# Kernel optimization log

Hardware: AMD Instinct MI355X
Metric: run time of the kernel (lower is better)

## Reference

```python
import jax, jax.numpy as jnp
import numpy as np

NP_, NA_ = 50000, 20000
D_IN, D_HID, D_OUT = 128, 128, 64
E_W, E_C, E_R = 250000, 500000, 250000


def setup_inputs() -> dict:
    key = jax.random.key(0)
    ks = jax.random.split(key, 14)
    s_in = 1.0 / np.sqrt(D_IN)
    s_h = 1.0 / np.sqrt(D_HID)
    return {
        "x_paper": jax.random.normal(ks[0], (NP_, D_IN), jnp.float32),
        "x_author": jax.random.normal(ks[1], (NA_, D_IN), jnp.float32),
        "Wl1": jax.random.normal(ks[2], (3, D_HID, D_IN), jnp.float32) * s_in,
        "bl1": jax.random.normal(ks[3], (3, D_HID), jnp.float32) * 0.01,
        "Wr1": jax.random.normal(ks[4], (3, D_HID, D_IN), jnp.float32) * s_in,
        "Wl2": jax.random.normal(ks[5], (3, D_OUT, D_HID), jnp.float32) * s_h,
        "bl2": jax.random.normal(ks[6], (3, D_OUT), jnp.float32) * 0.01,
        "Wr2": jax.random.normal(ks[7], (3, D_OUT, D_HID), jnp.float32) * s_h,
        "writes_src": jax.random.randint(ks[8], (E_W,), 0, NA_),
        "writes_dst": jax.random.randint(ks[9], (E_W,), 0, NP_),
        "cites_src": jax.random.randint(ks[10], (E_C,), 0, NP_),
        "cites_dst": jax.random.randint(ks[11], (E_C,), 0, NP_),
        "rev_src": jax.random.randint(ks[12], (E_R,), 0, NP_),
        "rev_dst": jax.random.randint(ks[13], (E_R,), 0, NA_),
    }


def _sage(x_src, x_dst, src, dst, Wl, bl, Wr, n_dst):
    # PyG SAGEConv(aggr='mean'): lin_l(mean_j x_src[j]) + lin_r(x_dst)
    agg = jax.ops.segment_sum(x_src[src], dst, num_segments=n_dst)
    cnt = jax.ops.segment_sum(jnp.ones_like(dst, dtype=x_src.dtype), dst,
                              num_segments=n_dst)
    agg = agg / jnp.maximum(cnt, 1.0)[:, None]  # degree-0 nodes -> 0 (PyG scatter-mean)
    return agg @ Wl.T + bl + x_dst @ Wr.T


def reference(x_paper, x_author, Wl1, bl1, Wr1, Wl2, bl2, Wr2,
              writes_src, writes_dst, cites_src, cites_dst, rev_src, rev_dst):
    def hetero_layer(xp, xa, Wl, bl, Wr):
        # HeteroConv(aggr='mean'): average per-relation outputs per dst node type
        op = 0.5 * (_sage(xa, xp, writes_src, writes_dst, Wl[0], bl[0], Wr[0], NP_)
                    + _sage(xp, xp, cites_src, cites_dst, Wl[1], bl[1], Wr[1], NP_))
        oa = _sage(xp, xa, rev_src, rev_dst, Wl[2], bl[2], Wr[2], NA_)
        return op, oa

    hp, ha = hetero_layer(x_paper, x_author, Wl1, bl1, Wr1)
    hp, ha = jax.nn.relu(hp), jax.nn.relu(ha)  # norm_type='none', dropout eval-mode
    hp, _ = hetero_layer(hp, ha, Wl2, bl2, Wr2)
    return hp  # logits for category='paper', [NP_, D_OUT]
```

## Files before the change

### kernel.cpp

```cpp
#include <hip/hip_runtime.h>

#define NP 50000
#define NA 20000
#define E_W 250000
#define E_C 500000
#define E_R 250000
#define E_TOT (E_W + E_C + E_R)
#define CAP 48
#define RBLK 4096
#define NSEG 245
#define PNODES 15000
#define CHK 125
#define NCH 120
#define NBIN 960

typedef __attribute__((ext_vector_type(8))) short short8;
typedef __attribute__((ext_vector_type(4))) float floatx4;
typedef __attribute__((ext_vector_type(2))) float floatx2;

__device__ __forceinline__ unsigned short f2bf(float f) {
    unsigned u = __float_as_uint(f);
    return (unsigned short)((u + 0x7FFFu + ((u >> 16) & 1u)) >> 16);
}
__device__ __forceinline__ float bflo(unsigned v) { return __uint_as_float(v << 16); }
__device__ __forceinline__ float bfhi(unsigned v) { return __uint_as_float(v & 0xFFFF0000u); }

__device__ __forceinline__ int frag_off(int NT, int j, int n, int k) {
    int t = n >> 4, ln = n & 15;
    int kb = k >> 5, q = (k >> 3) & 3, r = k & 7;
    return (((j * NT + t) * 4 + kb) * 64 + q * 16 + ln) * 8 + r;
}

__device__ __forceinline__ void prep_body(
    int idx,
    const float* __restrict__ xp, const float* __restrict__ xa,
    const float* __restrict__ Wl1, const float* __restrict__ Wr1,
    const float* __restrict__ Wl2, const float* __restrict__ Wr2,
    const float* __restrict__ bl1, const float* __restrict__ bl2,
    unsigned short* __restrict__ xpb, unsigned short* __restrict__ xab,
    unsigned* __restrict__ xp8, unsigned* __restrict__ xa8,
    unsigned short* __restrict__ Wp1, unsigned short* __restrict__ Wa1,
    unsigned short* __restrict__ Wt2, unsigned short* __restrict__ Wr2s,
    float* __restrict__ bias_p1, float* __restrict__ bias_a1,
    float* __restrict__ bias_p2) {
    const int n4p = NP * 32, n4a = NA * 32;
    if (idx < n4p + n4a) {
        const float* s; unsigned short* d; unsigned* d8; int i = idx;
        if (i < n4p) { s = xp; d = xpb; d8 = xp8; }
        else { s = xa; d = xab; d8 = xa8; i -= n4p; }
        float4 v = ((const float4*)s)[i];
        ushort4 u;
        u.x = f2bf(v.x); u.y = f2bf(v.y); u.z = f2bf(v.z); u.w = f2bf(v.w);
        ((ushort4*)d)[i] = u;
        int w = __builtin_amdgcn_cvt_pk_fp8_f32(v.x, v.y, 0, false);
        w = __builtin_amdgcn_cvt_pk_fp8_f32(v.z, v.w, w, true);
        d8[i] = (unsigned)w;
        return;
    }
    int j = idx - (n4p + n4a);
    if (j < 49152) {
        int jj = j >> 14, rem = j & 16383, n = rem >> 7, k = rem & 127;
        float v = (jj == 0)   ? 0.5f * Wl1[rem]
                  : (jj == 1) ? 0.5f * Wl1[16384 + rem]
                              : 0.5f * (Wr1[rem] + Wr1[16384 + rem]);
        Wp1[frag_off(8, jj, n, k)] = f2bf(v);
    } else if (j < 81920) {
        int i2 = j - 49152;
        int jj = i2 >> 14, rem = i2 & 16383, n = rem >> 7, k = rem & 127;
        float v = (jj == 0) ? Wl1[2 * 16384 + rem] : Wr1[2 * 16384 + rem];
        Wa1[frag_off(8, jj, n, k)] = f2bf(v);
    } else if (j < 98304) {
        int i2 = j - 81920;
        int jj = i2 >> 13, rem = i2 & 8191, n = rem >> 7, k = rem & 127;
        float v = 0.5f * Wl2[jj * 8192 + rem];
        Wt2[frag_off(4, jj, n, k)] = f2bf(v);
    } else if (j < 106496) {
        int i2 = j - 98304;
        int n = i2 >> 7, k = i2 & 127;
        float v = 0.5f * (Wr2[i2] + Wr2[8192 + i2]);
        Wr2s[frag_off(4, 0, n, k)] = f2bf(v);
    } else if (j < 106496 + 320) {
        int b = j - 106496;
        if (b < 128) bias_p1[b] = 0.5f * (bl1[b] + bl1[128 + b]);
        else if (b < 256) bias_a1[b - 128] = bl1[256 + b - 128];
        else bias_p2[b - 256] = 0.5f * (bl2[b - 256] + bl2[64 + b - 256]);
    }
}

__device__ __forceinline__ void edge_bin(
    int e, const int* __restrict__ w_src, const int* __restrict__ w_dst,
    const int* __restrict__ c_src, const int* __restrict__ c_dst,
    const int* __restrict__ r_src, const int* __restrict__ r_dst,
    int& bin, int& sub, int& src) {
    bool isC = (e >= E_W) & (e < E_W + E_C);
    bool isR = e >= E_W + E_C;
    const int* db = isR ? r_dst : (isC ? c_dst : w_dst);
    const int* sb = isR ? r_src : (isC ? c_src : w_src);
    int idx = e - (isC ? E_W : 0) - (isR ? (E_W + E_C) : 0);
    int d = db[idx];
    src = sb[idx];
    int p, local;
    if (isR) { p = d / 2500; local = 12500 + d - p * 2500; }
    else { p = d / 6250; local = (d - p * 6250) + (isC ? 6250 : 0); }
    int ch = local / CHK;
    bin = p * NCH + ch;
    sub = local - ch * CHK;
}

__device__ __forceinline__ void route_body(
    int bid, const int* __restrict__ w_src, const int* __restrict__ w_dst,
    const int* __restrict__ c_src, const int* __restrict__ c_dst,
    const int* __restrict__ r_src, const int* __restrict__ r_dst,
    unsigned* __restrict__ seg, int* __restrict__ segoff, int* __restrict__ segcnt,
    int* cnt_s, int* base_s, int* cur_s) {
    int tid = threadIdx.x, lane = tid & 63;
    for (int k = tid; k < NBIN; k += 256) cnt_s[k] = 0;
    __syncthreads();
#pragma unroll 4
    for (int u = 0; u < 16; ++u) {
        int e = bid * RBLK + u * 256 + tid;
        if (e < E_TOT) {
            int bin, sub, src;
            edge_bin(e, w_src, w_dst, c_src, c_dst, r_src, r_dst, bin, sub, src);
            atomicAdd(&cnt_s[bin], 1);
        }
    }
    __syncthreads();
    if (tid < 64) {
        int v[15], tot = 0;
#pragma unroll
        for (int q = 0; q < 15; ++q) {
            v[q] = cnt_s[tid * 15 + q];
            tot += v[q];
        }
        int sc = tot;
#pragma unroll
        for (int ofs = 1; ofs < 64; ofs <<= 1) {
            int t = __shfl_up(sc, ofs, 64);
            if (lane >= ofs) sc += t;
        }
        int run = sc - tot;
#pragma unroll
        for (int q = 0; q < 15; ++q) {
            base_s[tid * 15 + q] = run;
            run += v[q];
        }
    }
    __syncthreads();
    for (int k = tid; k < NBIN; k += 256) {
        segoff[bid * NBIN + k] = base_s[k];
        segcnt[bid * NBIN + k] = cnt_s[k];
        cur_s[k] = base_s[k];
    }
    __syncthreads();
    unsigned* segb = seg + (size_t)bid * RBLK;
#pragma unroll 4
    for (int u = 0; u < 16; ++u) {
        int e = bid * RBLK + u * 256 + tid;
        if (e < E_TOT) {
            int bin, sub, src;
            edge_bin(e, w_src, w_dst, c_src, c_dst, r_src, r_dst, bin, sub, src);
            int pos = atomicAdd(&cur_s[bin], 1);
            segb[pos] = (unsigned)src | ((unsigned)sub << 16);
        }
    }
}

__global__ __launch_bounds__(256) void route_prep(
    const float* xp, const float* xa, const float* Wl1, const float* Wr1,
    const float* Wl2, const float* Wr2, const float* bl1, const float* bl2,
    unsigned short* xpb, unsigned short* xab, unsigned* xp8, unsigned* xa8,
    unsigned short* Wp1, unsigned short* Wa1, unsigned short* Wt2, unsigned short* Wr2s,
    float* bias_p1, float* bias_a1, float* bias_p2,
    const int* w_src, const int* w_dst, const int* c_src, const int* c_dst,
    const int* r_src, const int* r_dst,
    unsigned* seg, int* segoff, int* segcnt) {
    __shared__ int cnt_s[NBIN], base_s[NBIN], cur_s[NBIN];
    if ((int)blockIdx.x < NSEG)
        route_body(blockIdx.x, w_src, w_dst, c_src, c_dst, r_src, r_dst,
                   seg, segoff, segcnt, cnt_s, base_s, cur_s);
    else
        prep_body((blockIdx.x - NSEG) * 256 + threadIdx.x, xp, xa, Wl1, Wr1, Wl2, Wr2,
                  bl1, bl2, xpb, xab, xp8, xa8, Wp1, Wa1, Wt2, Wr2s,
                  bias_p1, bias_a1, bias_p2);
}

__global__ __launch_bounds__(512) void fill_agg(
    const unsigned* __restrict__ seg, const int* __restrict__ segoff,
    const int* __restrict__ segcnt, int* __restrict__ cnt,
    unsigned short* __restrict__ csr,
    const unsigned* __restrict__ xp8, const unsigned* __restrict__ xa8,
    unsigned short* __restrict__ aggP1, unsigned short* __restrict__ aggP2,
    unsigned short* __restrict__ aggA) {
    __shared__ __align__(16) unsigned short rows[CHK * CAP];
    __shared__ int cursor[CHK];
    __shared__ int offs[NSEG], cnts[NSEG];
    int tid = threadIdx.x;
    int b = blockIdx.x, p, ch;
    if (b < 160)      { p = b / 20;  ch = 100 + b % 20; }
    else if (b < 560) { int t = b - 160; p = t / 50; ch = 50 + t % 50; }
    else              { int t = b - 560; p = t / 50; ch = t % 50; }
    int k = p * NCH + ch;
    for (int s = tid; s < NSEG; s += 512) {
        offs[s] = segoff[s * NBIN + k];
        cnts[s] = segcnt[s * NBIN + k];
    }
    for (int l = tid; l < CHK; l += 512) cursor[l] = 0;
    __syncthreads();
    int grp = tid >> 4, gl = tid & 15;
    for (int s = grp; s < NSEG; s += 32) {
        int n = cnts[s];
        const unsigned* sp = seg + (size_t)s * RBLK + offs[s];
        for (int i = gl; i < n; i += 16) {
            unsigned v = sp[i];
            int sub = v >> 16, src = v & 0xFFFFu;
            int pos = atomicAdd(&cursor[sub], 1);
            if (pos < CAP) rows[sub * CAP + pos] = (unsigned short)src;
        }
    }
    __syncthreads();
    if (ch < 100) {
        int gbase = p * PNODES + ch * CHK;
        for (int l = tid; l < CHK; l += 512) cnt[gbase + l] = cursor[l];
        const unsigned* rU = (const unsigned*)rows;
        unsigned* cU = (unsigned*)csr + (size_t)gbase * (CAP / 2);
        for (int i = tid; i < CHK * (CAP / 2); i += 512) cU[i] = rU[i];
    }
    const unsigned* src8; unsigned short* dst; int nodebase, dummy;
    if (ch < 50)       { src8 = xa8; dst = aggP1; nodebase = p * 6250 + ch * CHK;         dummy = NA; }
    else if (ch < 100) { src8 = xp8; dst = aggP2; nodebase = p * 6250 + (ch - 50) * CHK;  dummy = NP; }
    else               { src8 = xp8; dst = aggA;  nodebase = p * 2500 + (ch - 100) * CHK; dummy = NP; }
    int g = tid >> 5, sl = tid & 31;
    for (int l = g; l < CHK; l += 16) {
        int deg = cursor[l];
        int degc = deg < CAP ? deg : CAP;
        float a0 = 0.f, a1 = 0.f, a2 = 0.f, a3 = 0.f;
        float b0 = 0.f, b1 = 0.f, b2 = 0.f, b3 = 0.f;
        for (int i = 0; i < degc; i += 8) {
            short8 rr = *(const short8*)&rows[l * CAP + i];
            unsigned v[8];
#pragma unroll
            for (int u = 0; u < 8; ++u) {
                int ii = i + u;
                int q = (ii < degc) ? (int)(unsigned short)rr[u] : dummy;
                v[u] = src8[(q << 5) + sl];
            }
#pragma unroll
            for (int u = 0; u < 8; ++u) {
                floatx2 lo = __builtin_amdgcn_cvt_pk_f32_fp8(v[u], false);
                floatx2 hi = __builtin_amdgcn_cvt_pk_f32_fp8(v[u], true);
                if (u & 1) { b0 += lo.x; b1 += lo.y; b2 += hi.x; b3 += hi.y; }
                else       { a0 += lo.x; a1 += lo.y; a2 += hi.x; a3 += hi.y; }
            }
        }
        float scl = deg > 0 ? 1.f / (float)deg : 0.f;
        float r0 = (a0 + b0) * scl, r1 = (a1 + b1) * scl;
        float r2 = (a2 + b2) * scl, r3 = (a3 + b3) * scl;
        unsigned wlo = ((unsigned)f2bf(r1) << 16) | (unsigned)f2bf(r0);
        unsigned whi = ((unsigned)f2bf(r3) << 16) | (unsigned)f2bf(r2);
        ((uint2*)dst)[((nodebase + l) << 5) + sl] = make_uint2(wlo, whi);
    }
}

__global__ void agg2(const unsigned short* __restrict__ ta, const unsigned short* __restrict__ tp,
                     const int* __restrict__ cnt, const unsigned short* __restrict__ csr,
                     const float* __restrict__ sp_in, const float* __restrict__ bias_p2,
                     float* __restrict__ out) {
    int node = blockIdx.x * 8 + (threadIdx.x >> 5);
    if (node >= NP) return;
    int lane = threadIdx.x & 63;
    int sl = lane & 31;
    int hw = lane & 32;
    int p2 = node / 6250;
    int base = p2 * PNODES + (node - p2 * 6250);
    float r0 = 0.f, r1 = 0.f;
#pragma unroll
    for (int rel = 0; rel < 2; ++rel) {
        int dummy = (rel == 0) ? NA : NP;
        const unsigned* sp = (const unsigned*)((rel == 0) ? ta : tp);
        int idx = base + (rel ? 6250 : 0);
        int deg = cnt[idx];
        int degc = deg < CAP ? deg : CAP;
        const unsigned short* row = csr + (size_t)idx * CAP;
        int ei0 = (sl < degc) ? (int)row[sl] : dummy;
        int ei1 = (32 + sl < degc) ? (int)row[32 + sl] : dummy;
        int degw = degc;
        int other = __shfl_xor(degw, 32, 64);
        if (other > degw) degw = other;
        float s0 = 0.f, s1 = 0.f, t0 = 0.f, t1 = 0.f;
        for (int i = 0; i < degw; i += 8) {
            unsigned v[8];
#pragma unroll
            for (int u = 0; u < 8; ++u) {
                int ii = i + u;
                int esrc = (ii < 32) ? ei0 : ei1;
                int qq = __shfl(esrc, hw | (ii & 31), 64);
                qq = (ii < degc) ? qq : dummy;
                v[u] = sp[(qq << 5) + sl];
            }
#pragma unroll
            for (int u = 0; u < 8; ++u) {
                if (u & 1) { t0 += bflo(v[u]); t1 += bfhi(v[u]); }
                else       { s0 += bflo(v[u]); s1 += bfhi(v[u]); }
            }
        }
        float scl = deg > 0 ? 1.f / (float)deg : 0.f;
        r0 += (s0 + t0) * scl; r1 += (s1 + t1) * scl;
    }
    float2 spv = ((const float2*)sp_in)[(size_t)node * 32 + sl];
    float2 bv = ((const float2*)bias_p2)[sl];
    ((float2*)out)[(size_t)node * 32 + sl] =
        make_float2(r0 + spv.x + bv.x, r1 + spv.y + bv.y);
}

template <int J, bool SP>
__device__ __forceinline__ void l1_core(
    const unsigned short* __restrict__ A0, const unsigned short* __restrict__ A1,
    const unsigned short* __restrict__ A2, const unsigned short* __restrict__ Wf,
    const float* __restrict__ bias,
    const unsigned short* __restrict__ Wt, unsigned short* __restrict__ tout,
    const unsigned short* __restrict__ Wsp, float* __restrict__ spout,
    unsigned short (*hT)[136], int M, int blk) {
    int tid = threadIdx.x;
    int wave = tid >> 6, lane = tid & 63;
    int ln = lane & 15, quad = lane >> 4;
    int row = blk * 64 + wave * 16 + ln;
    int rowc = row < M ? row : M - 1;
    const unsigned short* As[3] = {A0, A1, A2};
    floatx4 acc[8];
#pragma unroll
    for (int t = 0; t < 8; ++t) acc[t] = (floatx4){0.f, 0.f, 0.f, 0.f};
#pragma unroll
    for (int j = 0; j < J; ++j) {
        const unsigned short* A = As[j] + (long)rowc * 128 + quad * 8;
        const unsigned short* Wj = Wf + j * (128 * 128) + lane * 8;
#pragma unroll
        for (int kb = 0; kb < 4; ++kb) {
            short8 af = *(const short8*)(A + kb * 32);
#pragma unroll
            for (int t = 0; t < 8; ++t) {
                short8 bf = *(const short8*)(Wj + (t * 4 + kb) * 512);
                acc[t] = __builtin_amdgcn_mfma_f32_16x16x32_bf16(af, bf, acc[t], 0, 0, 0);
            }
        }
    }
    int orow0 = blk * 64 + wave * 16 + quad * 4;
    int lrow0 = wave * 16 + quad * 4;
#pragma unroll
    for (int t = 0; t < 8; ++t) {
        int col = t * 16 + ln;
        float bv = bias[col];
#pragma unroll
        for (int r = 0; r < 4; ++r) {
            float v = fmaxf(acc[t][r] + bv, 0.f);
            hT[lrow0 + r][col] = f2bf(v);
        }
    }
    __syncthreads();
    floatx4 tacc[4], sacc[4];
#pragma unroll
    for (int t = 0; t < 4; ++t) {
        tacc[t] = (floatx4){0.f, 0.f, 0.f, 0.f};
        sacc[t] = (floatx4){0.f, 0.f, 0.f, 0.f};
    }
#pragma unroll
    for (int kb = 0; kb < 4; ++kb) {
        short8 af = *(const short8*)&hT[wave * 16 + ln][quad * 8 + kb * 32];
#pragma unroll
        for (int t = 0; t < 4; ++t) {
            short8 bf = *(const short8*)(Wt + (t * 4 + kb) * 512 + lane * 8);
            tacc[t] = __builtin_amdgcn_mfma_f32_16x16x32_bf16(af, bf, tacc[t], 0, 0, 0);
            if (SP) {
                short8 bs = *(const short8*)(Wsp + (t * 4 + kb) * 512 + lane * 8);
                sacc[t] = __builtin_amdgcn_mfma_f32_16x16x32_bf16(af, bs, sacc[t], 0, 0, 0);
            }
        }
    }
#pragma unroll
    for (int t = 0; t < 4; ++t) {
        int col = t * 16 + ln;
#pragma unroll
        for (int r = 0; r < 4; ++r) {
            int orow = orow0 + r;
            if (orow < M) {
                tout[(long)orow * 64 + col] = f2bf(tacc[t][r]);
                if (SP) spout[(long)orow * 64 + col] = sacc[t][r];
            }
        }
    }
}

__global__ __launch_bounds__(256) void gemm_l1f(
    const unsigned short* aggP1, const unsigned short* aggP2, const unsigned short* xpb,
    const unsigned short* Wp1, const float* bias_p1,
    const unsigned short* aggA, const unsigned short* xab,
    const unsigned short* Wa1, const float* bias_a1,
    const unsigned short* Wt2, const unsigned short* Wr2s,
    unsigned short* ta, unsigned short* tp, float* sp) {
    __shared__ unsigned short hT[64][136];
    constexpr int PB = (NP + 63) / 64;
    if ((int)blockIdx.x < PB)
        l1_core<3, true>(aggP1, aggP2, xpb, Wp1, bias_p1, Wt2 + 64 * 128, tp, Wr2s, sp,
                         hT, NP, blockIdx.x);
    else
        l1_core<2, false>(aggA, xab, nullptr, Wa1, bias_a1, Wt2, ta, nullptr, nullptr,
                          hT, NA, blockIdx.x - PB);
}

extern "C" void kernel_launch(void* const* d_in, const int* in_sizes, int n_in,
                              void* d_out, int out_size, void* d_ws, size_t ws_size,
                              hipStream_t stream) {
    (void)in_sizes; (void)n_in; (void)out_size; (void)ws_size;
    const float* xp  = (const float*)d_in[0];
    const float* xa  = (const float*)d_in[1];
    const float* Wl1 = (const float*)d_in[2];
    const float* bl1 = (const float*)d_in[3];
    const float* Wr1 = (const float*)d_in[4];
    const float* Wl2 = (const float*)d_in[5];
    const float* bl2 = (const float*)d_in[6];
    const float* Wr2 = (const float*)d_in[7];
    const int* w_src = (const int*)d_in[8];
    const int* w_dst = (const int*)d_in[9];
    const int* c_src = (const int*)d_in[10];
    const int* c_dst = (const int*)d_in[11];
    const int* r_src = (const int*)d_in[12];
    const int* r_dst = (const int*)d_in[13];
    float* out = (float*)d_out;

    char* p = (char*)d_ws;
    auto alloc = [&](size_t bytes) {
        char* r = p;
        p += (bytes + 255) & ~(size_t)255;
        return r;
    };
    unsigned short* xpb   = (unsigned short*)alloc((size_t)NP * 128 * 2);
    unsigned short* xab   = (unsigned short*)alloc((size_t)NA * 128 * 2);
    unsigned*       xp8   = (unsigned*)alloc((size_t)(NP + 1) * 128);
    unsigned*       xa8   = (unsigned*)alloc((size_t)(NA + 1) * 128);
    unsigned short* aggP1 = (unsigned short*)alloc((size_t)NP * 128 * 2);
    unsigned short* aggP2 = (unsigned short*)alloc((size_t)NP * 128 * 2);
    unsigned short* aggA  = (unsigned short*)alloc((size_t)NA * 128 * 2);
    unsigned short* ta    = (unsigned short*)alloc((size_t)(NA + 1) * 64 * 2);
    unsigned short* tp    = (unsigned short*)alloc((size_t)(NP + 1) * 64 * 2);
    float*          sp    = (float*)alloc((size_t)NP * 64 * 4);
    int*            cnt    = (int*)alloc((size_t)8 * PNODES * 4);
    unsigned short* csr    = (unsigned short*)alloc((size_t)8 * PNODES * CAP * 2);
    unsigned*       seg    = (unsigned*)alloc((size_t)NSEG * RBLK * 4);
    int*            segoff = (int*)alloc((size_t)NSEG * NBIN * 4);
    int*            segcnt = (int*)alloc((size_t)NSEG * NBIN * 4);
    unsigned short* Wp1  = (unsigned short*)alloc(3 * 128 * 128 * 2);
    unsigned short* Wa1  = (unsigned short*)alloc(2 * 128 * 128 * 2);
    unsigned short* Wt2  = (unsigned short*)alloc(2 * 64 * 128 * 2);
    unsigned short* Wr2s = (unsigned short*)alloc(64 * 128 * 2);
    float* bias_p1 = (float*)alloc(128 * 4);
    float* bias_a1 = (float*)alloc(128 * 4);
    float* bias_p2 = (float*)alloc(64 * 4);

    hipMemsetAsync(xp8 + (size_t)NP * 32, 0, 128, stream);
    hipMemsetAsync(xa8 + (size_t)NA * 32, 0, 128, stream);
    hipMemsetAsync(ta + (size_t)NA * 64, 0, 128, stream);
    hipMemsetAsync(tp + (size_t)NP * 64, 0, 128, stream);

    int prep_threads = (NP + NA) * 32 + 106496 + 320;
    int prep_blocks = (prep_threads + 255) / 256;
    route_prep<<<NSEG + prep_blocks, 256, 0, stream>>>(
        xp, xa, Wl1, Wr1, Wl2, Wr2, bl1, bl2,
        xpb, xab, xp8, xa8, Wp1, Wa1, Wt2, Wr2s, bias_p1, bias_a1, bias_p2,
        w_src, w_dst, c_src, c_dst, r_src, r_dst, seg, segoff, segcnt);

    fill_agg<<<NBIN, 512, 0, stream>>>(seg, segoff, segcnt, cnt, csr,
                                       xp8, xa8, aggP1, aggP2, aggA);

    gemm_l1f<<<(NP + 63) / 64 + (NA + 63) / 64, 256, 0, stream>>>(
        aggP1, aggP2, xpb, Wp1, bias_p1, aggA, xab, Wa1, bias_a1, Wt2, Wr2s, ta, tp, sp);

    agg2<<<(NP + 7) / 8, 256, 0, stream>>>(ta, tp, cnt, csr, sp, bias_p2, out);
}
```

Baseline: 207.7 us.

## Fuse layer-1 neighbor gather with layer-1 GEMM and layer-2 projection per 64-node tile

```diff
diff --git a/kernel.cpp b/kernel.cpp
--- a/kernel.cpp
+++ b/kernel.cpp
@@ -9,10 +9,9 @@
 #define CAP 48
 #define RBLK 4096
 #define NSEG 245
-#define PNODES 15000
-#define CHK 125
-#define NCH 120
-#define NBIN 960
+#define NCHP 782
+#define NCHA 313
+#define NBIN (NCHP + NCHA)
 
 typedef __attribute__((ext_vector_type(8))) short short8;
 typedef __attribute__((ext_vector_type(4))) float floatx4;
@@ -99,12 +98,8 @@
     int idx = e - (isC ? E_W : 0) - (isR ? (E_W + E_C) : 0);
     int d = db[idx];
     src = sb[idx];
-    int p, local;
-    if (isR) { p = d / 2500; local = 12500 + d - p * 2500; }
-    else { p = d / 6250; local = (d - p * 6250) + (isC ? 6250 : 0); }
-    int ch = local / CHK;
-    bin = p * NCH + ch;
-    sub = local - ch * CHK;
+    if (isR) { bin = NCHP + (d >> 6); sub = d & 63; }
+    else { bin = d >> 6; sub = (d & 63) + (isC ? 64 : 0); }
 }
 
 __device__ __forceinline__ void route_body(
@@ -127,10 +122,11 @@
     }
     __syncthreads();
     if (tid < 64) {
-        int v[15], tot = 0;
-#pragma unroll
-        for (int q = 0; q < 15; ++q) {
-            v[q] = cnt_s[tid * 15 + q];
+        int v[18], tot = 0;
+#pragma unroll
+        for (int q = 0; q < 18; ++q) {
+            int k = tid * 18 + q;
+            v[q] = (k < NBIN) ? cnt_s[k] : 0;
             tot += v[q];
         }
         int sc = tot;
@@ -141,9 +137,9 @@
         }
         int run = sc - tot;
 #pragma unroll
-        for (int q = 0; q < 15; ++q) {
-            base_s[tid * 15 + q] = run;
-            run += v[q];
+        for (int q = 0; q < 18; ++q) {
+            int k = tid * 18 + q;
+            if (k < NBIN) { base_s[k] = run; run += v[q]; }
         }
     }
     __syncthreads();
@@ -185,80 +181,201 @@
                   bias_p1, bias_a1, bias_p2);
 }
 
-__global__ __launch_bounds__(512) void fill_agg(
+__global__ __launch_bounds__(512) void fill_l1(
     const unsigned* __restrict__ seg, const int* __restrict__ segoff,
     const int* __restrict__ segcnt, int* __restrict__ cnt,
     unsigned short* __restrict__ csr,
     const unsigned* __restrict__ xp8, const unsigned* __restrict__ xa8,
-    unsigned short* __restrict__ aggP1, unsigned short* __restrict__ aggP2,
-    unsigned short* __restrict__ aggA) {
-    __shared__ __align__(16) unsigned short rows[CHK * CAP];
-    __shared__ int cursor[CHK];
+    const unsigned short* __restrict__ xpb, const unsigned short* __restrict__ xab,
+    const unsigned short* __restrict__ Wp1, const float* __restrict__ bias_p1,
+    const unsigned short* __restrict__ Wa1, const float* __restrict__ bias_a1,
+    const unsigned short* __restrict__ Wt2, const unsigned short* __restrict__ Wr2s,
+    unsigned short* __restrict__ ta, unsigned short* __restrict__ tp,
+    float* __restrict__ sp) {
+    __shared__ unsigned short rows[128 * CAP];
+    __shared__ int cursor[128];
     __shared__ int offs[NSEG], cnts[NSEG];
+    __shared__ __align__(16) unsigned short aggL[64][136];
     int tid = threadIdx.x;
-    int b = blockIdx.x, p, ch;
-    if (b < 160)      { p = b / 20;  ch = 100 + b % 20; }
-    else if (b < 560) { int t = b - 160; p = t / 50; ch = 50 + t % 50; }
-    else              { int t = b - 560; p = t / 50; ch = t % 50; }
-    int k = p * NCH + ch;
+    int k = blockIdx.x;
+    bool isPaper = k < NCHP;
+    int base = isPaper ? k * 64 : (k - NCHP) * 64;
+    int total = isPaper ? NP : NA;
+    int M = total - base; if (M > 64) M = 64;
+
     for (int s = tid; s < NSEG; s += 512) {
         offs[s] = segoff[s * NBIN + k];
         cnts[s] = segcnt[s * NBIN + k];
     }
-    for (int l = tid; l < CHK; l += 512) cursor[l] = 0;
-    __syncthreads();
-    int grp = tid >> 4, gl = tid & 15;
-    for (int s = grp; s < NSEG; s += 32) {
-        int n = cnts[s];
-        const unsigned* sp = seg + (size_t)s * RBLK + offs[s];
-        for (int i = gl; i < n; i += 16) {
-            unsigned v = sp[i];
-            int sub = v >> 16, src = v & 0xFFFFu;
-            int pos = atomicAdd(&cursor[sub], 1);
-            if (pos < CAP) rows[sub * CAP + pos] = (unsigned short)src;
-        }
-    }
-    __syncthreads();
-    if (ch < 100) {
-        int gbase = p * PNODES + ch * CHK;
-        for (int l = tid; l < CHK; l += 512) cnt[gbase + l] = cursor[l];
+    if (tid < 128) cursor[tid] = 0;
+    __syncthreads();
+    {
+        int grp = tid >> 4, gl = tid & 15;
+        for (int s = grp; s < NSEG; s += 32) {
+            int n = cnts[s];
+            const unsigned* spq = seg + (size_t)s * RBLK + offs[s];
+            for (int i = gl; i < n; i += 16) {
+                unsigned v = spq[i];
+                int sub = v >> 16, srcn = v & 0xFFFFu;
+                int pos = atomicAdd(&cursor[sub], 1);
+                if (pos < CAP) rows[sub * CAP + pos] = (unsigned short)srcn;
+            }
+        }
+    }
+    __syncthreads();
+    if (isPaper) {
+        for (int r = tid; r < 2 * M; r += 512)
+            cnt[base * 2 + r] = cursor[(r >> 1) + ((r & 1) << 6)];
         const unsigned* rU = (const unsigned*)rows;
-        unsigned* cU = (unsigned*)csr + (size_t)gbase * (CAP / 2);
-        for (int i = tid; i < CHK * (CAP / 2); i += 512) cU[i] = rU[i];
-    }
-    const unsigned* src8; unsigned short* dst; int nodebase, dummy;
-    if (ch < 50)       { src8 = xa8; dst = aggP1; nodebase = p * 6250 + ch * CHK;         dummy = NA; }
-    else if (ch < 100) { src8 = xp8; dst = aggP2; nodebase = p * 6250 + (ch - 50) * CHK;  dummy = NP; }
-    else               { src8 = xp8; dst = aggA;  nodebase = p * 2500 + (ch - 100) * CHK; dummy = NP; }
-    int g = tid >> 5, sl = tid & 31;
-    for (int l = g; l < CHK; l += 16) {
-        int deg = cursor[l];
-        int degc = deg < CAP ? deg : CAP;
-        float a0 = 0.f, a1 = 0.f, a2 = 0.f, a3 = 0.f;
-        float b0 = 0.f, b1 = 0.f, b2 = 0.f, b3 = 0.f;
-        for (int i = 0; i < degc; i += 8) {
-            short8 rr = *(const short8*)&rows[l * CAP + i];
-            unsigned v[8];
-#pragma unroll
-            for (int u = 0; u < 8; ++u) {
-                int ii = i + u;
-                int q = (ii < degc) ? (int)(unsigned short)rr[u] : dummy;
-                v[u] = src8[(q << 5) + sl];
-            }
-#pragma unroll
-            for (int u = 0; u < 8; ++u) {
-                floatx2 lo = __builtin_amdgcn_cvt_pk_f32_fp8(v[u], false);
-                floatx2 hi = __builtin_amdgcn_cvt_pk_f32_fp8(v[u], true);
-                if (u & 1) { b0 += lo.x; b1 += lo.y; b2 += hi.x; b3 += hi.y; }
-                else       { a0 += lo.x; a1 += lo.y; a2 += hi.x; a3 += hi.y; }
-            }
-        }
-        float scl = deg > 0 ? 1.f / (float)deg : 0.f;
-        float r0 = (a0 + b0) * scl, r1 = (a1 + b1) * scl;
-        float r2 = (a2 + b2) * scl, r3 = (a3 + b3) * scl;
-        unsigned wlo = ((unsigned)f2bf(r1) << 16) | (unsigned)f2bf(r0);
-        unsigned whi = ((unsigned)f2bf(r3) << 16) | (unsigned)f2bf(r2);
-        ((uint2*)dst)[((nodebase + l) << 5) + sl] = make_uint2(wlo, whi);
+        unsigned* cU = (unsigned*)csr + (size_t)base * 2 * (CAP / 2);
+        for (int i = tid; i < 2 * M * (CAP / 2); i += 512) {
+            int r = i / (CAP / 2), j = i - r * (CAP / 2);
+            cU[i] = rU[((r >> 1) + ((r & 1) << 6)) * (CAP / 2) + j];
+        }
+    }
+
+    int wave = tid >> 6, lane = tid & 63, ln = lane & 15, quad = lane >> 4;
+    int wrow = (wave & 3) * 16, nhalf = wave >> 2;
+    floatx4 acc[4];
+#pragma unroll
+    for (int t = 0; t < 4; ++t) acc[t] = (floatx4){0.f, 0.f, 0.f, 0.f};
+
+    auto gather = [&](int rel, const unsigned* __restrict__ src8, int dummy) {
+        int g = tid >> 5, sl = tid & 31;
+        for (int l = g; l < 64; l += 16) {
+            int deg = cursor[l + (rel << 6)];
+            int degc = deg < CAP ? deg : CAP;
+            const unsigned short* rp = &rows[(l + (rel << 6)) * CAP];
+            float a0 = 0.f, a1 = 0.f, a2 = 0.f, a3 = 0.f;
+            float b0 = 0.f, b1 = 0.f, b2 = 0.f, b3 = 0.f;
+            for (int i = 0; i < degc; i += 8) {
+                short8 rr = *(const short8*)&rp[i];
+                unsigned v[8];
+#pragma unroll
+                for (int u = 0; u < 8; ++u) {
+                    int ii = i + u;
+                    int q = (ii < degc) ? (int)(unsigned short)rr[u] : dummy;
+                    v[u] = src8[(q << 5) + sl];
+                }
+#pragma unroll
+                for (int u = 0; u < 8; ++u) {
+                    floatx2 lo = __builtin_amdgcn_cvt_pk_f32_fp8(v[u], false);
+                    floatx2 hi = __builtin_amdgcn_cvt_pk_f32_fp8(v[u], true);
+                    if (u & 1) { b0 += lo.x; b1 += lo.y; b2 += hi.x; b3 += hi.y; }
+                    else       { a0 += lo.x; a1 += lo.y; a2 += hi.x; a3 += hi.y; }
+                }
+            }
+            float scl = deg > 0 ? 1.f / (float)deg : 0.f;
+            float r0 = (a0 + b0) * scl, r1 = (a1 + b1) * scl;
+            float r2 = (a2 + b2) * scl, r3 = (a3 + b3) * scl;
+            unsigned wlo = ((unsigned)f2bf(r1) << 16) | (unsigned)f2bf(r0);
+            unsigned whi = ((unsigned)f2bf(r3) << 16) | (unsigned)f2bf(r2);
+            *(uint2*)&aggL[l][sl * 4] = make_uint2(wlo, whi);
+        }
+    };
+    auto gemm_lds = [&](const unsigned short* __restrict__ Wb) {
+#pragma unroll
+        for (int kb = 0; kb < 4; ++kb) {
+            short8 af = *(const short8*)&aggL[wrow + ln][quad * 8 + kb * 32];
+#pragma unroll
+            for (int t = 0; t < 4; ++t) {
+                short8 bf = *(const short8*)(Wb + ((nhalf * 4 + t) * 4 + kb) * 512 + lane * 8);
+                acc[t] = __builtin_amdgcn_mfma_f32_16x16x32_bf16(af, bf, acc[t], 0, 0, 0);
+            }
+        }
+    };
+    auto gemm_glob = [&](const unsigned short* __restrict__ X,
+                         const unsigned short* __restrict__ Wb) {
+        int row = base + wrow + ln;
+        int rowc = row < total ? row : total - 1;
+        const unsigned short* A = X + (size_t)rowc * 128 + quad * 8;
+#pragma unroll
+        for (int kb = 0; kb < 4; ++kb) {
+            short8 af = *(const short8*)(A + kb * 32);
+#pragma unroll
+            for (int t = 0; t < 4; ++t) {
+                short8 bf = *(const short8*)(Wb + ((nhalf * 4 + t) * 4 + kb) * 512 + lane * 8);
+                acc[t] = __builtin_amdgcn_mfma_f32_16x16x32_bf16(af, bf, acc[t], 0, 0, 0);
+            }
+        }
+    };
+
+    if (isPaper) {
+        gather(0, xa8, NA);
+        __syncthreads();
+        gemm_lds(Wp1);
+        __syncthreads();
+        gather(1, xp8, NP);
+        __syncthreads();
+        gemm_lds(Wp1 + 16384);
+        gemm_glob(xpb, Wp1 + 2 * 16384);
+        __syncthreads();
+    } else {
+        gather(0, xp8, NP);
+        __syncthreads();
+        gemm_lds(Wa1);
+        gemm_glob(xab, Wa1 + 16384);
+        __syncthreads();
+    }
+    {
+        const float* bias = isPaper ? bias_p1 : bias_a1;
+#pragma unroll
+        for (int t = 0; t < 4; ++t) {
+            int col = nhalf * 64 + t * 16 + ln;
+            float bv = bias[col];
+#pragma unroll
+            for (int r = 0; r < 4; ++r)
+                aggL[wrow + quad * 4 + r][col] = f2bf(fmaxf(acc[t][r] + bv, 0.f));
+        }
+    }
+    __syncthreads();
+    floatx4 tacc[4];
+#pragma unroll
+    for (int t = 0; t < 4; ++t) tacc[t] = (floatx4){0.f, 0.f, 0.f, 0.f};
+    int rows16 = (wave & 3) * 16;
+    if (isPaper) {
+        const unsigned short* W = (wave < 4) ? (Wt2 + 64 * 128) : Wr2s;
+#pragma unroll
+        for (int kb = 0; kb < 4; ++kb) {
+            short8 af = *(const short8*)&aggL[rows16 + ln][quad * 8 + kb * 32];
+#pragma unroll
+            for (int t = 0; t < 4; ++t) {
+                short8 bf = *(const short8*)(W + (t * 4 + kb) * 512 + lane * 8);
+                tacc[t] = __builtin_amdgcn_mfma_f32_16x16x32_bf16(af, bf, tacc[t], 0, 0, 0);
+            }
+        }
+#pragma unroll
+        for (int t = 0; t < 4; ++t) {
+            int col = t * 16 + ln;
+#pragma unroll
+            for (int r = 0; r < 4; ++r) {
+                int lr = rows16 + quad * 4 + r;
+                if (lr < M) {
+                    if (wave < 4) tp[(size_t)(base + lr) * 64 + col] = f2bf(tacc[t][r]);
+                    else sp[(size_t)(base + lr) * 64 + col] = tacc[t][r];
+                }
+            }
+        }
+    } else {
+        int thalf = wave >> 2;
+#pragma unroll
+        for (int kb = 0; kb < 4; ++kb) {
+            short8 af = *(const short8*)&aggL[rows16 + ln][quad * 8 + kb * 32];
+#pragma unroll
+            for (int tt = 0; tt < 2; ++tt) {
+                short8 bf = *(const short8*)(Wt2 + ((thalf * 2 + tt) * 4 + kb) * 512 + lane * 8);
+                tacc[tt] = __builtin_amdgcn_mfma_f32_16x16x32_bf16(af, bf, tacc[tt], 0, 0, 0);
+            }
+        }
+#pragma unroll
+        for (int tt = 0; tt < 2; ++tt) {
+            int col = (thalf * 2 + tt) * 16 + ln;
+#pragma unroll
+            for (int r = 0; r < 4; ++r) {
+                int lr = rows16 + quad * 4 + r;
+                if (lr < M) ta[(size_t)(base + lr) * 64 + col] = f2bf(tacc[tt][r]);
+            }
+        }
     }
 }
 
@@ -271,14 +388,12 @@
     int lane = threadIdx.x & 63;
     int sl = lane & 31;
     int hw = lane & 32;
-    int p2 = node / 6250;
-    int base = p2 * PNODES + (node - p2 * 6250);
     float r0 = 0.f, r1 = 0.f;
 #pragma unroll
     for (int rel = 0; rel < 2; ++rel) {
         int dummy = (rel == 0) ? NA : NP;
         const unsigned* sp = (const unsigned*)((rel == 0) ? ta : tp);
-        int idx = base + (rel ? 6250 : 0);
+        int idx = node * 2 + rel;
         int deg = cnt[idx];
         int degc = deg < CAP ? deg : CAP;
         const unsigned short* row = csr + (size_t)idx * CAP;
@@ -311,100 +426,6 @@
     float2 bv = ((const float2*)bias_p2)[sl];
     ((float2*)out)[(size_t)node * 32 + sl] =
         make_float2(r0 + spv.x + bv.x, r1 + spv.y + bv.y);
-}
-
-template <int J, bool SP>
-__device__ __forceinline__ void l1_core(
-    const unsigned short* __restrict__ A0, const unsigned short* __restrict__ A1,
-    const unsigned short* __restrict__ A2, const unsigned short* __restrict__ Wf,
-    const float* __restrict__ bias,
-    const unsigned short* __restrict__ Wt, unsigned short* __restrict__ tout,
-    const unsigned short* __restrict__ Wsp, float* __restrict__ spout,
-    unsigned short (*hT)[136], int M, int blk) {
-    int tid = threadIdx.x;
-    int wave = tid >> 6, lane = tid & 63;
-    int ln = lane & 15, quad = lane >> 4;
-    int row = blk * 64 + wave * 16 + ln;
-    int rowc = row < M ? row : M - 1;
-    const unsigned short* As[3] = {A0, A1, A2};
-    floatx4 acc[8];
-#pragma unroll
-    for (int t = 0; t < 8; ++t) acc[t] = (floatx4){0.f, 0.f, 0.f, 0.f};
-#pragma unroll
-    for (int j = 0; j < J; ++j) {
-        const unsigned short* A = As[j] + (long)rowc * 128 + quad * 8;
-        const unsigned short* Wj = Wf + j * (128 * 128) + lane * 8;
-#pragma unroll
-        for (int kb = 0; kb < 4; ++kb) {
-            short8 af = *(const short8*)(A + kb * 32);
-#pragma unroll
-            for (int t = 0; t < 8; ++t) {
-                short8 bf = *(const short8*)(Wj + (t * 4 + kb) * 512);
-                acc[t] = __builtin_amdgcn_mfma_f32_16x16x32_bf16(af, bf, acc[t], 0, 0, 0);
-            }
-        }
-    }
-    int orow0 = blk * 64 + wave * 16 + quad * 4;
-    int lrow0 = wave * 16 + quad * 4;
-#pragma unroll
-    for (int t = 0; t < 8; ++t) {
-        int col = t * 16 + ln;
-        float bv = bias[col];
-#pragma unroll
-        for (int r = 0; r < 4; ++r) {
-            float v = fmaxf(acc[t][r] + bv, 0.f);
-            hT[lrow0 + r][col] = f2bf(v);
-        }
-    }
-    __syncthreads();
-    floatx4 tacc[4], sacc[4];
-#pragma unroll
-    for (int t = 0; t < 4; ++t) {
-        tacc[t] = (floatx4){0.f, 0.f, 0.f, 0.f};
-        sacc[t] = (floatx4){0.f, 0.f, 0.f, 0.f};
-    }
-#pragma unroll
-    for (int kb = 0; kb < 4; ++kb) {
-        short8 af = *(const short8*)&hT[wave * 16 + ln][quad * 8 + kb * 32];
-#pragma unroll
-        for (int t = 0; t < 4; ++t) {
-            short8 bf = *(const short8*)(Wt + (t * 4 + kb) * 512 + lane * 8);
-            tacc[t] = __builtin_amdgcn_mfma_f32_16x16x32_bf16(af, bf, tacc[t], 0, 0, 0);
-            if (SP) {
-                short8 bs = *(const short8*)(Wsp + (t * 4 + kb) * 512 + lane * 8);
-                sacc[t] = __builtin_amdgcn_mfma_f32_16x16x32_bf16(af, bs, sacc[t], 0, 0, 0);
-            }
-        }
-    }
-#pragma unroll
-    for (int t = 0; t < 4; ++t) {
-        int col = t * 16 + ln;
-#pragma unroll
-        for (int r = 0; r < 4; ++r) {
-            int orow = orow0 + r;
-            if (orow < M) {
-                tout[(long)orow * 64 + col] = f2bf(tacc[t][r]);
-                if (SP) spout[(long)orow * 64 + col] = sacc[t][r];
-            }
-        }
-    }
-}
-
-__global__ __launch_bounds__(256) void gemm_l1f(
-    const unsigned short* aggP1, const unsigned short* aggP2, const unsigned short* xpb,
-    const unsigned short* Wp1, const float* bias_p1,
-    const unsigned short* aggA, const unsigned short* xab,
-    const unsigned short* Wa1, const float* bias_a1,
-    const unsigned short* Wt2, const unsigned short* Wr2s,
-    unsigned short* ta, unsigned short* tp, float* sp) {
-    __shared__ unsigned short hT[64][136];
-    constexpr int PB = (NP + 63) / 64;
-    if ((int)blockIdx.x < PB)
-        l1_core<3, true>(aggP1, aggP2, xpb, Wp1, bias_p1, Wt2 + 64 * 128, tp, Wr2s, sp,
-                         hT, NP, blockIdx.x);
-    else
-        l1_core<2, false>(aggA, xab, nullptr, Wa1, bias_a1, Wt2, ta, nullptr, nullptr,
-                          hT, NA, blockIdx.x - PB);
 }
 
 extern "C" void kernel_launch(void* const* d_in, const int* in_sizes, int n_in,
@@ -437,14 +458,11 @@
     unsigned short* xab   = (unsigned short*)alloc((size_t)NA * 128 * 2);
     unsigned*       xp8   = (unsigned*)alloc((size_t)(NP + 1) * 128);
     unsigned*       xa8   = (unsigned*)alloc((size_t)(NA + 1) * 128);
-    unsigned short* aggP1 = (unsigned short*)alloc((size_t)NP * 128 * 2);
-    unsigned short* aggP2 = (unsigned short*)alloc((size_t)NP * 128 * 2);
-    unsigned short* aggA  = (unsigned short*)alloc((size_t)NA * 128 * 2);
     unsigned short* ta    = (unsigned short*)alloc((size_t)(NA + 1) * 64 * 2);
     unsigned short* tp    = (unsigned short*)alloc((size_t)(NP + 1) * 64 * 2);
     float*          sp    = (float*)alloc((size_t)NP * 64 * 4);
-    int*            cnt    = (int*)alloc((size_t)8 * PNODES * 4);
-    unsigned short* csr    = (unsigned short*)alloc((size_t)8 * PNODES * CAP * 2);
+    int*            cnt    = (int*)alloc((size_t)NP * 2 * 4);
+    unsigned short* csr    = (unsigned short*)alloc((size_t)NP * 2 * CAP * 2);
     unsigned*       seg    = (unsigned*)alloc((size_t)NSEG * RBLK * 4);
     int*            segoff = (int*)alloc((size_t)NSEG * NBIN * 4);
     int*            segcnt = (int*)alloc((size_t)NSEG * NBIN * 4);
@@ -468,11 +486,9 @@
         xpb, xab, xp8, xa8, Wp1, Wa1, Wt2, Wr2s, bias_p1, bias_a1, bias_p2,
         w_src, w_dst, c_src, c_dst, r_src, r_dst, seg, segoff, segcnt);
 
-    fill_agg<<<NBIN, 512, 0, stream>>>(seg, segoff, segcnt, cnt, csr,
-                                       xp8, xa8, aggP1, aggP2, aggA);
-
-    gemm_l1f<<<(NP + 63) / 64 + (NA + 63) / 64, 256, 0, stream>>>(
-        aggP1, aggP2, xpb, Wp1, bias_p1, aggA, xab, Wa1, bias_a1, Wt2, Wr2s, ta, tp, sp);
+    fill_l1<<<NBIN, 512, 0, stream>>>(seg, segoff, segcnt, cnt, csr,
+                                      xp8, xa8, xpb, xab, Wp1, bias_p1, Wa1, bias_a1,
+                                      Wt2, Wr2s, ta, tp, sp);
 
     agg2<<<(NP + 7) / 8, 256, 0, stream>>>(ta, tp, cnt, csr, sp, bias_p2, out);
 }
```

Result: faster. 199.1 us (-4.1%).
